# Kernel tuning notes

Hardware: AMD Instinct MI355X
Metric: run time of the kernel (lower is better)

The kernel has to match this reference:

```python
import jax, jax.numpy as jnp
import numpy as np

N = 8192
IN_FEATS = 256
D = IN_FEATS // 4  # 64, bottleneck dim
HID = 64           # MLP hidden_dim
K_MAX = 9
K_EC = 20
SLOPE = 0.01       # torch LeakyReLU default


def _leaky(x):
    return jnp.where(x >= 0, x, SLOPE * x)


def _knn_idx(f, k):
    # f: [N, d]; returns [N, k] indices of k nearest (incl. self, dist 0), ascending distance
    sq = jnp.sum(f * f, axis=1)
    dist = sq[:, None] + sq[None, :] - 2.0 * (f @ f.T)  # [N, N]
    _, idx = jax.lax.top_k(-dist, k)
    return idx


def _edge_conv(f, idx, Wt, bt, Wp, bp, W1, b1, W2, b2):
    # f: [N, d]; idx: [N, k] neighbor (src) indices; dst is the row node.
    x_nb = f[idx]                                   # [N, k, d] gather of src feats
    theta = (f[:, None, :] - x_nb) @ Wt.T + bt      # v_sub_u -> theta Linear
    phi = f @ Wp.T + bp                             # [N, d]
    z = phi[:, None, :] + theta                     # [N, k, d]
    # MLP(hidden=64, 2 layers, leaky_relu, activation_first=True)
    z = _leaky(z) @ W1.T + b1
    z = _leaky(z) @ W2.T + b2
    return jnp.max(z, axis=1)                       # max aggregation per dst


def _lin_init(key, out_dim, in_dim):
    k1, k2 = jax.random.split(key)
    bound = 1.0 / np.sqrt(in_dim)
    W = jax.random.uniform(k1, (out_dim, in_dim), jnp.float32, -bound, bound)
    b = jax.random.uniform(k2, (out_dim,), jnp.float32, -bound, bound)
    return W, b


def setup_inputs() -> dict:
    key = jax.random.key(0)
    keys = jax.random.split(key, 12)
    inp = {"feature": jax.random.normal(keys[0], (N, IN_FEATS), jnp.float32)}
    inp["Wb"], inp["bb"] = _lin_init(keys[1], D, IN_FEATS)
    inp["Wt1"], inp["bt1"] = _lin_init(keys[2], D, D)
    inp["Wp1"], inp["bp1"] = _lin_init(keys[3], D, D)
    inp["Wm1a"], inp["bm1a"] = _lin_init(keys[4], HID, D)
    inp["Wm1b"], inp["bm1b"] = _lin_init(keys[5], D, HID)
    inp["Wt2"], inp["bt2"] = _lin_init(keys[6], D, D)
    inp["Wp2"], inp["bp2"] = _lin_init(keys[7], D, D)
    inp["Wm2a"], inp["bm2a"] = _lin_init(keys[8], HID, D)
    inp["Wm2b"], inp["bm2b"] = _lin_init(keys[9], D, HID)
    inp["Wl"], inp["bl"] = _lin_init(keys[10], IN_FEATS, 3 * D)
    return inp


def reference(feature, Wb, bb, Wt1, bt1, Wp1, bp1, Wm1a, bm1a, Wm1b, bm1b,
              Wt2, bt2, Wp2, bp2, Wm2a, bm2a, Wm2b, bm2b, Wl, bl):
    f = feature @ Wb.T + bb                          # bottleneck [N, D]
    # KNN indices are non-differentiable (torch topk indices) -> stop_gradient
    idx40 = _knn_idx(jax.lax.stop_gradient(f), K_EC * 2)  # 40-NN, ascending distance
    idx9 = idx40[:, :K_MAX]
    idx20 = idx40[:, :K_EC]            # dilation 1
    idx20_d2 = idx40[:, ::2]           # dilation 2: every 2nd of 40-NN
    h_max = jnp.max(f[idx9], axis=1)   # copy_u + max over 9-NN
    h1 = _edge_conv(f, idx20, Wt1, bt1, Wp1, bp1, Wm1a, bm1a, Wm1b, bm1b)
    h2 = _edge_conv(f, idx20_d2, Wt2, bt2, Wp2, bp2, Wm2a, bm2a, Wm2b, bm2b)
    h = jnp.concatenate([h1, h2, h_max], axis=1) @ Wl.T + bl
    return h + feature                 # residual
```

## Files before the change

kernel.cpp:

```cpp
#include <hip/hip_runtime.h>
#include <math.h>

#define NPT   8192
#define FIN   256
#define DD    64
#define KSEL  48
#define SSEG  320

#define LEAKY(x) (((x) >= 0.f) ? (x) : 0.01f*(x))

using short8v = __attribute__((ext_vector_type(8))) short;
using f32x4   = __attribute__((ext_vector_type(4))) float;

__device__ inline unsigned short f2bf(float x) {
  union { float f; unsigned u; } v; v.f = x;
  unsigned r = v.u + 0x7fff + ((v.u >> 16) & 1);
  return (unsigned short)(r >> 16);
}
__device__ inline float bf2f(unsigned short h) {
  union { unsigned u; float f; } v; v.u = ((unsigned)h) << 16; return v.f;
}
__device__ inline unsigned key_of(float f) {
  unsigned u = __float_as_uint(f);
  return (u & 0x80000000u) ? ~u : (u | 0x80000000u);
}
__device__ inline float key_inv(unsigned k) {
  unsigned u = (k >> 31) ? (k ^ 0x80000000u) : ~k;
  return __uint_as_float(u);
}

__global__ void k0_prep(const float* __restrict__ Wl, const float* __restrict__ Wb,
                        const float* __restrict__ Wt1, const float* __restrict__ Wp1,
                        const float* __restrict__ Wt2, const float* __restrict__ Wp2,
                        float* __restrict__ WlT, float* __restrict__ WbT,
                        float* __restrict__ WtT1, float* __restrict__ WpT1,
                        float* __restrict__ WtT2, float* __restrict__ WpT2)
{
  const int b = blockIdx.x, t = threadIdx.x;
  if (b < 192) {
    WlT[b*256 + t] = Wl[t*192 + b];
  } else if (b < 256) {
    int j = (b - 192)*4 + (t >> 6), o = t & 63;
    WbT[j*64 + o] = Wb[o*256 + j];
  } else {
    int m = b - 256;
    const float* src = (m==0) ? Wt1 : (m==1) ? Wp1 : (m==2) ? Wt2 : Wp2;
    float*       dst = (m==0) ? WtT1: (m==1) ? WpT1: (m==2) ? WtT2: WpT2;
    #pragma unroll
    for (int i = 0; i < 16; ++i) {
      int idx = t + 256*i, r = idx >> 6, c = idx & 63;
      dst[c*64 + r] = src[r*64 + c];
    }
  }
}

__global__ __launch_bounds__(256) void k1_precompute(
    const float* __restrict__ feature, const float* __restrict__ WbT, const float* __restrict__ bb,
    const float* __restrict__ WtT1, const float* __restrict__ bt1,
    const float* __restrict__ WpT1, const float* __restrict__ bp1,
    const float* __restrict__ WtT2, const float* __restrict__ bt2,
    const float* __restrict__ WpT2, const float* __restrict__ bp2,
    double* __restrict__ f64d, double* __restrict__ sq64,
    float* __restrict__ f32v, float* __restrict__ sqf,
    float* __restrict__ u1, float* __restrict__ c1,
    float* __restrict__ u2, float* __restrict__ c2)
{
  __shared__ float f_s[4*64];
  const int w = threadIdx.x >> 6, l = threadIdx.x & 63;
  const int i = blockIdx.x*4 + w;
  const float* frow = feature + i*FIN;
  double a0 = (double)bb[l], a1 = 0.0, a2 = 0.0, a3 = 0.0;
  #pragma unroll 2
  for (int j = 0; j < FIN; j += 4) {
    float4 fv = *(const float4*)&frow[j];
    a0 += (double)fv.x * (double)WbT[(j+0)*64 + l];
    a1 += (double)fv.y * (double)WbT[(j+1)*64 + l];
    a2 += (double)fv.z * (double)WbT[(j+2)*64 + l];
    a3 += (double)fv.w * (double)WbT[(j+3)*64 + l];
  }
  double facc = (a0 + a1) + (a2 + a3);
  f64d[i*DD + l] = facc;
  float f32 = (float)facc;
  f32v[i*DD + l] = f32;
  double s = facc*facc;
  #pragma unroll
  for (int off = 32; off; off >>= 1) s += __shfl_xor(s, off);
  if (l == 0) { sq64[i] = s; sqf[i] = (float)s; }
  f_s[w*64 + l] = f32;
  float au1 = 0.f, ap1 = 0.f, au2 = 0.f, ap2 = 0.f;
  for (int e = 0; e < DD; ++e) {
    float fe = f_s[w*64 + e];
    au1 += fe * WtT1[e*64 + l];
    ap1 += fe * WpT1[e*64 + l];
    au2 += fe * WtT2[e*64 + l];
    ap2 += fe * WpT2[e*64 + l];
  }
  u1[i*DD+l] = au1;
  c1[i*DD+l] = ap1 + bp1[l] + au1 + bt1[l];
  u2[i*DD+l] = au2;
  c2[i*DD+l] = ap2 + bp2[l] + au2 + bt2[l];
}

__global__ __launch_bounds__(256) void k1b_frag(
    const float* __restrict__ f32v,
    unsigned short* __restrict__ Saf, unsigned short* __restrict__ Sbf)
{
  const int w = threadIdx.x >> 6, l = threadIdx.x & 63;
  const int task = blockIdx.x*4 + w;
  const int tile = task / 6, ks = task % 6;
  const int row  = tile*16 + (l & 15);
  const int inner = (ks & 1)*32 + ((l >> 4) << 3);
  union { unsigned short u[8]; short8v v; } pa, pb;
  #pragma unroll
  for (int j = 0; j < 8; ++j) {
    float x = f32v[row*64 + inner + j];
    unsigned short hi = f2bf(x);
    unsigned short lo = f2bf(x - bf2f(hi));
    pa.u[j] = (ks < 4) ? hi : lo;
    pb.u[j] = (ks < 2) ? hi : ((ks < 4) ? lo : hi);
  }
  size_t off = ((size_t)(tile*6 + ks)*64 + l)*8;
  *(short8v*)&Saf[off] = pa.v;
  *(short8v*)&Sbf[off] = pb.v;
}

__global__ __launch_bounds__(256) void k1c_wfrag(
    const float* __restrict__ Wm1a, const float* __restrict__ Wm1b,
    const float* __restrict__ Wm2a, const float* __restrict__ Wm2b,
    unsigned short* __restrict__ F1a, unsigned short* __restrict__ F1b,
    unsigned short* __restrict__ F2a, unsigned short* __restrict__ F2b)
{
  const int w = threadIdx.x >> 6, l = threadIdx.x & 63;
  const int task = blockIdx.x*4 + w;
  const int which = task / 24, rem = task % 24;
  const int nt = rem / 6, ks = rem % 6;
  const float* W = (which==0) ? Wm1a : (which==1) ? Wm1b : (which==2) ? Wm2a : Wm2b;
  unsigned short* F = (which==0) ? F1a : (which==1) ? F1b : (which==2) ? F2a : F2b;
  const int row = nt*16 + (l & 15);
  const int inner = (ks & 1)*32 + ((l >> 4) << 3);
  union { unsigned short u[8]; short8v v; } p;
  #pragma unroll
  for (int j = 0; j < 8; ++j) {
    float x = W[row*64 + inner + j];
    unsigned short hi = f2bf(x);
    unsigned short lo = f2bf(x - bf2f(hi));
    p.u[j] = (ks < 2) ? hi : ((ks < 4) ? lo : hi);
  }
  *(short8v*)&F[((size_t)(nt*6 + ks)*64 + l)*8] = p.v;
}

#define MFMA_PAIR6(ACC, AF, BF)                                                  \
  ACC = __builtin_amdgcn_mfma_f32_16x16x32_bf16(AF[0], BF[0], ACC, 0, 0, 0);     \
  ACC = __builtin_amdgcn_mfma_f32_16x16x32_bf16(AF[1], BF[1], ACC, 0, 0, 0);     \
  ACC = __builtin_amdgcn_mfma_f32_16x16x32_bf16(AF[0], BF[2], ACC, 0, 0, 0);     \
  ACC = __builtin_amdgcn_mfma_f32_16x16x32_bf16(AF[1], BF[3], ACC, 0, 0, 0);     \
  ACC = __builtin_amdgcn_mfma_f32_16x16x32_bf16(AF[2], BF[0], ACC, 0, 0, 0);     \
  ACC = __builtin_amdgcn_mfma_f32_16x16x32_bf16(AF[3], BF[1], ACC, 0, 0, 0);

__global__ __launch_bounds__(512) void k2a_sample(
    const unsigned short* __restrict__ Saf,
    const unsigned short* __restrict__ Sbf,
    const float* __restrict__ sqf,
    float* __restrict__ sampD)
{
  const int t = threadIdx.x, w = t >> 6, l = t & 63;
  const int qb = blockIdx.x >> 1, sh = blockIdx.x & 1;
  const int qbase = qb * 32;
  short8v afr[2][4];
  #pragma unroll
  for (int mt = 0; mt < 2; ++mt) {
    const size_t b = (size_t)(qb*2 + mt)*6;
    afr[mt][0] = *(const short8v*)&Saf[((b+0)*64 + l)*8];
    afr[mt][1] = *(const short8v*)&Saf[((b+1)*64 + l)*8];
    afr[mt][2] = *(const short8v*)&Saf[((b+4)*64 + l)*8];
    afr[mt][3] = *(const short8v*)&Saf[((b+5)*64 + l)*8];
  }
  const int ncol = w*16 + (l & 15);
  for (int sl = 0; sl < 4; ++sl) {
    const int s = sh*4 + sl;
    const int cb = s*8;
    const int jbase = cb*128;
    short8v bfr[4];
    {
      const size_t b = (size_t)(cb*8 + w)*6;
      #pragma unroll
      for (int k = 0; k < 4; ++k)
        bfr[k] = *(const short8v*)&Sbf[((b+k)*64 + l)*8];
    }
    const float sc = sqf[jbase + ncol];
    f32x4 acc0 = {0.f,0.f,0.f,0.f}, acc1 = {0.f,0.f,0.f,0.f};
    MFMA_PAIR6(acc0, afr[0], bfr);
    MFMA_PAIR6(acc1, afr[1], bfr);
    #pragma unroll
    for (int r = 0; r < 4; ++r) {
      const int q0 = qbase + 0*16 + (l >> 4)*4 + r;
      const int q1 = qbase + 1*16 + (l >> 4)*4 + r;
      sampD[(size_t)q0*1024 + s*128 + ncol] = sc - 2.0f*acc0[r];
      sampD[(size_t)q1*1024 + s*128 + ncol] = sc - 2.0f*acc1[r];
    }
  }
}

__global__ __launch_bounds__(256) void k2t_threshold(
    const float* __restrict__ sampD, float* __restrict__ Tq)
{
  const int w = threadIdx.x >> 6, l = threadIdx.x & 63;
  const int q = blockIdx.x*4 + w;
  unsigned ku[16];
  #pragma unroll
  for (int k = 0; k < 16; ++k)
    ku[k] = key_of(sampD[(size_t)q*1024 + k*64 + l]);
  unsigned prefix = 0; int need = 41;
  for (int b = 31; b >= 0; --b) {
    unsigned p2 = prefix << 1;
    int c = 0;
    #pragma unroll
    for (int k = 0; k < 16; ++k) c += ((ku[k] >> b) == p2);
    #pragma unroll
    for (int off = 32; off; off >>= 1) c += __shfl_xor(c, off);
    if (c >= need) prefix = p2; else { prefix = p2 | 1u; need -= c; }
  }
  if (l == 0) Tq[q] = key_inv(prefix);
}

__global__ __launch_bounds__(512) void k2f_filter(
    const unsigned short* __restrict__ Saf,
    const unsigned short* __restrict__ Sbf,
    const float* __restrict__ sqf,
    const float* __restrict__ Tq,
    int* __restrict__ cnt_g,
    float* __restrict__ survD, int* __restrict__ survI)
{
  __shared__ int cnt_sh[32];
  const int t = threadIdx.x, w = t >> 6, l = t & 63;
  const int qb = blockIdx.x >> 1, half = blockIdx.x & 1;
  const int qbase = qb * 32;
  if (t < 32) cnt_sh[t] = 0;
  short8v afr[2][4];
  float Tr[2][4]; int qloc[2][4];
  #pragma unroll
  for (int mt = 0; mt < 2; ++mt) {
    const size_t b = (size_t)(qb*2 + mt)*6;
    afr[mt][0] = *(const short8v*)&Saf[((b+0)*64 + l)*8];
    afr[mt][1] = *(const short8v*)&Saf[((b+1)*64 + l)*8];
    afr[mt][2] = *(const short8v*)&Saf[((b+4)*64 + l)*8];
    afr[mt][3] = *(const short8v*)&Saf[((b+5)*64 + l)*8];
    #pragma unroll
    for (int r = 0; r < 4; ++r) {
      qloc[mt][r] = mt*16 + (l >> 4)*4 + r;
      Tr[mt][r] = Tq[qbase + qloc[mt][r]];
    }
  }
  short8v bfr[4];
  {
    const size_t b = (size_t)(half*256 + w)*6;
    #pragma unroll
    for (int k = 0; k < 4; ++k)
      bfr[k] = *(const short8v*)&Sbf[((b+k)*64 + l)*8];
  }
  const int ncol = w*16 + (l & 15);
  __syncthreads();
  for (int cb = 0; cb < 32; ++cb) {
    const int jbase = half*4096 + cb*128;
    const float sc = sqf[jbase + ncol];
    f32x4 acc0 = {0.f,0.f,0.f,0.f}, acc1 = {0.f,0.f,0.f,0.f};
    MFMA_PAIR6(acc0, afr[0], bfr);
    MFMA_PAIR6(acc1, afr[1], bfr);
    if (cb < 31) {
      const size_t b = (size_t)(half*256 + (cb+1)*8 + w)*6;
      #pragma unroll
      for (int k = 0; k < 4; ++k)
        bfr[k] = *(const short8v*)&Sbf[((b+k)*64 + l)*8];
    }
    const int j = jbase + ncol;
    #pragma unroll
    for (int r = 0; r < 4; ++r) {
      float d0 = sc - 2.0f*acc0[r];
      if (d0 < Tr[0][r]) {
        int slot = atomicAdd(&cnt_sh[qloc[0][r]], 1);
        if (slot < SSEG) {
          size_t base = ((size_t)(qbase + qloc[0][r])*2 + half)*SSEG + slot;
          survD[base] = d0; survI[base] = j;
        }
      }
      float d1 = sc - 2.0f*acc1[r];
      if (d1 < Tr[1][r]) {
        int slot = atomicAdd(&cnt_sh[qloc[1][r]], 1);
        if (slot < SSEG) {
          size_t base = ((size_t)(qbase + qloc[1][r])*2 + half)*SSEG + slot;
          survD[base] = d1; survI[base] = j;
        }
      }
    }
  }
  __syncthreads();
  if (t < 32) cnt_g[(qbase + t)*2 + half] = cnt_sh[t];
}

__global__ __launch_bounds__(256) void k2s_select(
    const float* __restrict__ survD, const int* __restrict__ survI,
    const int* __restrict__ cnt_g, int* __restrict__ idx48)
{
  const int w = threadIdx.x >> 6, l = threadIdx.x & 63;
  const int node = blockIdx.x*4 + w;
  const int c0 = min(cnt_g[node*2 + 0], SSEG);
  const int c1 = min(cnt_g[node*2 + 1], SSEG);
  unsigned ku[10]; int iv[10];
  #pragma unroll
  for (int k = 0; k < 10; ++k) {
    int e = k*64 + l;
    int seg = (e >= SSEG);
    int off = e - seg*SSEG;
    bool v = off < (seg ? c1 : c0);
    size_t base = ((size_t)node*2 + seg)*SSEG + off;
    float d = v ? survD[base] : 0.f;
    iv[k] = v ? survI[base] : 0;
    ku[k] = v ? key_of(d) : 0xFFFFFFFFu;
  }
  unsigned prefix = 0; int need = KSEL;
  for (int b = 31; b >= 0; --b) {
    unsigned p2 = prefix << 1;
    int c = 0;
    #pragma unroll
    for (int k = 0; k < 10; ++k) c += ((ku[k] >> b) == p2);
    #pragma unroll
    for (int off = 32; off; off >>= 1) c += __shfl_xor(c, off);
    if (c >= need) prefix = p2; else { prefix = p2 | 1u; need -= c; }
  }
  const unsigned long long below = (1ull << l) - 1ull;
  int base = 0;
  #pragma unroll
  for (int k = 0; k < 10; ++k) {
    unsigned long long blt = __ballot(ku[k] < prefix);
    if (ku[k] < prefix) {
      int pos = base + __popcll(blt & below);
      idx48[(size_t)node*KSEL + pos] = iv[k];
    }
    base += __popcll(blt);
  }
  #pragma unroll
  for (int k = 0; k < 10; ++k) {
    unsigned long long beq = __ballot(ku[k] == prefix);
    if (ku[k] == prefix) {
      int pos = base + __popcll(beq & below);
      if (pos < KSEL) idx48[(size_t)node*KSEL + pos] = iv[k];
    }
    base += __popcll(beq);
  }
}

__global__ __launch_bounds__(256) void k2r_rerank(
    const double* __restrict__ f64d, const double* __restrict__ sq64,
    const int* __restrict__ idx48, int* __restrict__ idx40)
{
  __shared__ double part[KSEL][4];
  __shared__ double dist_sh[KSEL];
  __shared__ int    cand_sh[KSEL];
  const int t = threadIdx.x;
  const int node = blockIdx.x;
  if (t < KSEL) cand_sh[t] = idx48[(size_t)node*KSEL + t];
  __syncthreads();
  if (t < 192) {
    int c = t >> 2, qt = t & 3;
    int cand = cand_sh[c];
    const double* fi = f64d + (size_t)node*DD + qt*16;
    const double* fc = f64d + (size_t)cand*DD + qt*16;
    double a0 = 0.0, a1 = 0.0;
    #pragma unroll
    for (int d = 0; d < 16; d += 2) { a0 += fi[d]*fc[d]; a1 += fi[d+1]*fc[d+1]; }
    part[c][qt] = a0 + a1;
  }
  __syncthreads();
  if (t < KSEL) {
    int cand = cand_sh[t];
    dist_sh[t] = sq64[node] + sq64[cand]
               - 2.0*(part[t][0] + part[t][1] + part[t][2] + part[t][3]);
  }
  __syncthreads();
  if (t < KSEL) {
    double dm = dist_sh[t]; int cand = cand_sh[t];
    int rank = 0;
    for (int j = 0; j < KSEL; ++j) {
      double dj = dist_sh[j];
      int    ij = cand_sh[j];
      rank += (dj < dm) || (dj == dm && ij < cand);
    }
    if (rank < 40) idx40[(size_t)node*40 + rank] = cand;
  }
}

__global__ __launch_bounds__(256) void k3_edgeconv(
    const float* __restrict__ f32v,
    const float* __restrict__ u1, const float* __restrict__ c1,
    const float* __restrict__ u2, const float* __restrict__ c2,
    const unsigned short* __restrict__ F1a, const unsigned short* __restrict__ F1b,
    const unsigned short* __restrict__ F2a, const unsigned short* __restrict__ F2b,
    const float* __restrict__ bm1a, const float* __restrict__ bm1b,
    const float* __restrict__ bm2a, const float* __restrict__ bm2b,
    const int* __restrict__ idx40, float* __restrict__ hout)
{
  __shared__ unsigned short au16[2][32*72];
  __shared__ float red_s[2][2][64];
  __shared__ int idx_sh[80];
  const int t = threadIdx.x;
  const int w = t >> 6, l = t & 63;
  const int sub = w >> 1, mt = w & 1;
  const int i = blockIdx.x*2 + sub;
  const int row16 = l & 15;
  const int q8 = (l >> 4) << 3;
  if (t < 80) idx_sh[t] = idx40[(size_t)(blockIdx.x*2 + (t >= 40))*40 + (t >= 40 ? t - 40 : t)];
  __syncthreads();

  for (int conv = 0; conv < 2; ++conv) {
    const float* u_g = conv ? u2 : u1;
    const float* c_g = conv ? c2 : c1;
    const unsigned short* WfA = conv ? F2a : F1a;
    const unsigned short* WfB = conv ? F2b : F1b;
    const float* bav = conv ? bm2a : bm1a;
    const float* bbv = conv ? bm2b : bm1b;

    const int row = mt*16 + row16;
    const bool valid = row < 20;
    const int nb = valid ? idx_sh[sub*40 + (conv ? 2*row : row)] : idx_sh[sub*40];
    short8v fr0, fr1;
    {
      const float* up = u_g + (size_t)nb*DD;
      const float* cp = c_g + (size_t)i*DD;
      float4 ua = *(const float4*)&up[q8];
      float4 ub = *(const float4*)&up[q8 + 4];
      float4 uc = *(const float4*)&up[32 + q8];
      float4 ud = *(const float4*)&up[32 + q8 + 4];
      float4 ca = *(const float4*)&cp[q8];
      float4 cb = *(const float4*)&cp[q8 + 4];
      float4 cc = *(const float4*)&cp[32 + q8];
      float4 cd = *(const float4*)&cp[32 + q8 + 4];
      float z0[8] = {ca.x-ua.x, ca.y-ua.y, ca.z-ua.z, ca.w-ua.w,
                     cb.x-ub.x, cb.y-ub.y, cb.z-ub.z, cb.w-ub.w};
      float z1[8] = {cc.x-uc.x, cc.y-uc.y, cc.z-uc.z, cc.w-uc.w,
                     cd.x-ud.x, cd.y-ud.y, cd.z-ud.z, cd.w-ud.w};
      union { unsigned short us[8]; short8v v; } h0, h1;
      #pragma unroll
      for (int j = 0; j < 8; ++j) {
        float x0 = valid ? LEAKY(z0[j]) : 0.f;
        float x1 = valid ? LEAKY(z1[j]) : 0.f;
        h0.us[j] = f2bf(x0);
        h1.us[j] = f2bf(x1);
      }
      fr0 = h0.v; fr1 = h1.v;
    }
    f32x4 acc[4] = {{0,0,0,0},{0,0,0,0},{0,0,0,0},{0,0,0,0}};
    #pragma unroll
    for (int nt = 0; nt < 4; ++nt) {
      const unsigned short* p = WfA + (size_t)nt*6*64*8;
      short8v w0 = *(const short8v*)&p[(0*64 + l)*8];
      short8v w1 = *(const short8v*)&p[(1*64 + l)*8];
      acc[nt] = __builtin_amdgcn_mfma_f32_16x16x32_bf16(fr0, w0, acc[nt], 0, 0, 0);
      acc[nt] = __builtin_amdgcn_mfma_f32_16x16x32_bf16(fr1, w1, acc[nt], 0, 0, 0);
    }
    #pragma unroll
    for (int nt = 0; nt < 4; ++nt) {
      const int col = nt*16 + row16;
      const float ba = bav[col];
      #pragma unroll
      for (int r = 0; r < 4; ++r) {
        const int arow = mt*16 + (l >> 4)*4 + r;
        float v = acc[nt][r] + ba; v = LEAKY(v);
        au16[sub][arow*72 + col] = f2bf(v);
      }
    }
    __syncthreads();
    short8v g0, g1;
    {
      const unsigned short* base = &au16[sub][(mt*16 + row16)*72 + q8];
      g0 = *(const short8v*)&base[0];
      g1 = *(const short8v*)&base[32];
    }
    f32x4 bacc[4] = {{0,0,0,0},{0,0,0,0},{0,0,0,0},{0,0,0,0}};
    #pragma unroll
    for (int nt = 0; nt < 4; ++nt) {
      const unsigned short* p = WfB + (size_t)nt*6*64*8;
      short8v w0 = *(const short8v*)&p[(0*64 + l)*8];
      short8v w1 = *(const short8v*)&p[(1*64 + l)*8];
      bacc[nt] = __builtin_amdgcn_mfma_f32_16x16x32_bf16(g0, w0, bacc[nt], 0, 0, 0);
      bacc[nt] = __builtin_amdgcn_mfma_f32_16x16x32_bf16(g1, w1, bacc[nt], 0, 0, 0);
    }
    #pragma unroll
    for (int nt = 0; nt < 4; ++nt) {
      const int col = nt*16 + row16;
      const float bb2 = bbv[col];
      float m = -__builtin_inff();
      #pragma unroll
      for (int r = 0; r < 4; ++r) {
        const int arow = mt*16 + (l >> 4)*4 + r;
        if (arow < 20) m = fmaxf(m, bacc[nt][r] + bb2);
      }
      m = fmaxf(m, __shfl_xor(m, 16));
      m = fmaxf(m, __shfl_xor(m, 32));
      if ((l >> 4) == 0) red_s[sub][mt][col] = m;
    }
    __syncthreads();
    if (t < 128) {
      int s2 = t >> 6, col = t & 63;
      hout[(size_t)(blockIdx.x*2 + s2)*192 + conv*64 + col] =
          fmaxf(red_s[s2][0][col], red_s[s2][1][col]);
    }
    __syncthreads();
  }
  if (t < 128) {
    int s2 = t >> 6, col = t & 63;
    float m = -__builtin_inff();
    #pragma unroll
    for (int k = 0; k < 9; ++k)
      m = fmaxf(m, f32v[(size_t)idx_sh[s2*40 + k]*DD + col]);
    hout[(size_t)(blockIdx.x*2 + s2)*192 + 128 + col] = m;
  }
}

__global__ __launch_bounds__(256) void k4_final(
    const float* __restrict__ hbuf, const float* __restrict__ WlT,
    const float* __restrict__ bl, const float* __restrict__ feature,
    float* __restrict__ out)
{
  __shared__ __align__(16) float h_sh[16*192];
  const int t = threadIdx.x;
  const int nbase = blockIdx.x * 16;
  #pragma unroll
  for (int r = 0; r < 3; ++r) {
    int flat = t + 256*r;
    int n = flat / 48, j4 = flat % 48;
    *(float4*)&h_sh[n*192 + 4*j4] = *(const float4*)&hbuf[(nbase+n)*192 + 4*j4];
  }
  __syncthreads();
  float acc[16];
  #pragma unroll
  for (int n = 0; n < 16; ++n) acc[n] = 0.f;
  for (int j4 = 0; j4 < 48; ++j4) {
    float w0 = WlT[(4*j4+0)*256 + t];
    float w1 = WlT[(4*j4+1)*256 + t];
    float w2 = WlT[(4*j4+2)*256 + t];
    float w3 = WlT[(4*j4+3)*256 + t];
    #pragma unroll
    for (int n = 0; n < 16; ++n) {
      float4 hv = *(const float4*)&h_sh[n*192 + 4*j4];
      acc[n] += hv.x*w0 + hv.y*w1 + hv.z*w2 + hv.w*w3;
    }
  }
  float blv = bl[t];
  #pragma unroll
  for (int n = 0; n < 16; ++n)
    out[(nbase+n)*256 + t] = acc[n] + blv + feature[(nbase+n)*256 + t];
}

extern "C" void kernel_launch(void* const* d_in, const int* in_sizes, int n_in,
                              void* d_out, int out_size, void* d_ws, size_t ws_size,
                              hipStream_t stream) {
  const float* feature = (const float*)d_in[0];
  const float* Wb   = (const float*)d_in[1];
  const float* bb   = (const float*)d_in[2];
  const float* Wt1  = (const float*)d_in[3];
  const float* bt1  = (const float*)d_in[4];
  const float* Wp1  = (const float*)d_in[5];
  const float* bp1  = (const float*)d_in[6];
  const float* Wm1a = (const float*)d_in[7];
  const float* bm1a = (const float*)d_in[8];
  const float* Wm1b = (const float*)d_in[9];
  const float* bm1b = (const float*)d_in[10];
  const float* Wt2  = (const float*)d_in[11];
  const float* bt2  = (const float*)d_in[12];
  const float* Wp2  = (const float*)d_in[13];
  const float* bp2  = (const float*)d_in[14];
  const float* Wm2a = (const float*)d_in[15];
  const float* bm2a = (const float*)d_in[16];
  const float* Wm2b = (const float*)d_in[17];
  const float* bm2b = (const float*)d_in[18];
  const float* Wl   = (const float*)d_in[19];
  const float* bl   = (const float*)d_in[20];
  float* out = (float*)d_out;

  char* ws = (char*)d_ws;
  double* f64d = (double*)(ws + 0);
  double* sq64 = (double*)(ws + 4194304);
  float*  f32v = (float*)(ws + 4259840);
  float*  sqf  = (float*)(ws + 6356992);
  float*  u1   = (float*)(ws + 6389760);
  float*  c1   = (float*)(ws + 8486912);
  float*  u2   = (float*)(ws + 10584064);
  float*  c2   = (float*)(ws + 12681216);
  int*    idx48= (int*)(ws + 14778368);
  int*    idx40= (int*)(ws + 16351232);
  float*  hbuf = (float*)(ws + 17661952);
  float*  WlT  = (float*)(ws + 23953408);
  unsigned short* Saf = (unsigned short*)(ws + 24150016);
  unsigned short* Sbf = (unsigned short*)(ws + 27295744);
  float*  WbT  = (float*)(ws + 30441472);
  float*  WtT1 = (float*)(ws + 30507008);
  float*  WpT1 = (float*)(ws + 30523392);
  float*  WtT2 = (float*)(ws + 30539776);
  float*  WpT2 = (float*)(ws + 30556160);
  unsigned short* F1a = (unsigned short*)(ws + 30572544);
  unsigned short* F1b = (unsigned short*)(ws + 30597120);
  unsigned short* F2a = (unsigned short*)(ws + 30621696);
  unsigned short* F2b = (unsigned short*)(ws + 30646272);
  float*  Tq   = (float*)(ws + 30670848);
  int*    cnt_g= (int*)(ws + 30703616);
  float*  survD= (float*)(ws + 30769152);
  int*    survI= (int*)(ws + 51740672);
  float*  sampD= (float*)(ws + 30769152);

  hipLaunchKernelGGL(k0_prep, dim3(260), dim3(256), 0, stream,
                     Wl, Wb, Wt1, Wp1, Wt2, Wp2, WlT, WbT, WtT1, WpT1, WtT2, WpT2);
  hipLaunchKernelGGL(k1c_wfrag, dim3(24), dim3(256), 0, stream,
                     Wm1a, Wm1b, Wm2a, Wm2b, F1a, F1b, F2a, F2b);
  hipLaunchKernelGGL(k1_precompute, dim3(2048), dim3(256), 0, stream,
                     feature, WbT, bb, WtT1, bt1, WpT1, bp1, WtT2, bt2, WpT2, bp2,
                     f64d, sq64, f32v, sqf, u1, c1, u2, c2);
  hipLaunchKernelGGL(k1b_frag, dim3(768), dim3(256), 0, stream, f32v, Saf, Sbf);
  hipLaunchKernelGGL(k2a_sample, dim3(512), dim3(512), 0, stream, Saf, Sbf, sqf, sampD);
  hipLaunchKernelGGL(k2t_threshold, dim3(2048), dim3(256), 0, stream, sampD, Tq);
  hipLaunchKernelGGL(k2f_filter, dim3(512), dim3(512), 0, stream,
                     Saf, Sbf, sqf, Tq, cnt_g, survD, survI);
  hipLaunchKernelGGL(k2s_select, dim3(2048), dim3(256), 0, stream, survD, survI, cnt_g, idx48);
  hipLaunchKernelGGL(k2r_rerank, dim3(8192), dim3(256), 0, stream, f64d, sq64, idx48, idx40);
  hipLaunchKernelGGL(k3_edgeconv, dim3(4096), dim3(256), 0, stream,
                     f32v, u1, c1, u2, c2, F1a, F1b, F2a, F2b,
                     bm1a, bm1b, bm2a, bm2b, idx40, hbuf);
  hipLaunchKernelGGL(k4_final, dim3(512), dim3(256), 0, stream, hbuf, WlT, bl, feature, out);
}
```

Measured before the change: 396.7 us.

## Split precompute: stage bottleneck weights in LDS, compute theta/phi projections via MFMA

The old fused precompute kernel is split in two. The new first kernel computes the f64 bottleneck projection with 8 rows per block and the WbT weights staged in shared memory as float4. The u/c projections (Wt and Wt+Wp, folded algebraically) now run as a bf16 hi/lo split MFMA kernel that reuses the Saf fragments, after the KNN stages. This replaces scalar fp32 FMA loops and their global weight reads with matrix-core work. The cost is some precision, since the split bf16 scheme drops the lo*lo terms, and the new G weight buffers alias the f64d workspace region, which is only safe because they are written after rerank.

```diff
diff --git a/kernel.cpp b/kernel.cpp
--- a/kernel.cpp
+++ b/kernel.cpp
@@ -30,75 +30,57 @@
 }
 
 __global__ void k0_prep(const float* __restrict__ Wl, const float* __restrict__ Wb,
-                        const float* __restrict__ Wt1, const float* __restrict__ Wp1,
-                        const float* __restrict__ Wt2, const float* __restrict__ Wp2,
-                        float* __restrict__ WlT, float* __restrict__ WbT,
-                        float* __restrict__ WtT1, float* __restrict__ WpT1,
-                        float* __restrict__ WtT2, float* __restrict__ WpT2)
+                        float* __restrict__ WlT, float* __restrict__ WbT)
 {
   const int b = blockIdx.x, t = threadIdx.x;
   if (b < 192) {
     WlT[b*256 + t] = Wl[t*192 + b];
-  } else if (b < 256) {
+  } else {
     int j = (b - 192)*4 + (t >> 6), o = t & 63;
     WbT[j*64 + o] = Wb[o*256 + j];
-  } else {
-    int m = b - 256;
-    const float* src = (m==0) ? Wt1 : (m==1) ? Wp1 : (m==2) ? Wt2 : Wp2;
-    float*       dst = (m==0) ? WtT1: (m==1) ? WpT1: (m==2) ? WtT2: WpT2;
-    #pragma unroll
-    for (int i = 0; i < 16; ++i) {
-      int idx = t + 256*i, r = idx >> 6, c = idx & 63;
-      dst[c*64 + r] = src[r*64 + c];
-    }
-  }
-}
-
-__global__ __launch_bounds__(256) void k1_precompute(
-    const float* __restrict__ feature, const float* __restrict__ WbT, const float* __restrict__ bb,
-    const float* __restrict__ WtT1, const float* __restrict__ bt1,
-    const float* __restrict__ WpT1, const float* __restrict__ bp1,
-    const float* __restrict__ WtT2, const float* __restrict__ bt2,
-    const float* __restrict__ WpT2, const float* __restrict__ bp2,
+  }
+}
+
+__global__ __launch_bounds__(512) void k1a_f64(
+    const float* __restrict__ feature, const float* __restrict__ WbT,
+    const float* __restrict__ bb,
     double* __restrict__ f64d, double* __restrict__ sq64,
-    float* __restrict__ f32v, float* __restrict__ sqf,
-    float* __restrict__ u1, float* __restrict__ c1,
-    float* __restrict__ u2, float* __restrict__ c2)
-{
-  __shared__ float f_s[4*64];
-  const int w = threadIdx.x >> 6, l = threadIdx.x & 63;
-  const int i = blockIdx.x*4 + w;
-  const float* frow = feature + i*FIN;
+    float* __restrict__ f32v, float* __restrict__ sqf)
+{
+  __shared__ __align__(16) float4 Q[64*64];
+  const int t = threadIdx.x, w = t >> 6, l = t & 63;
+  const int i = blockIdx.x*8 + w;
+  #pragma unroll
+  for (int r = 0; r < 8; ++r) {
+    int flat = t + 512*r;
+    int jj = flat >> 6, col = flat & 63;
+    float4 q;
+    q.x = WbT[(4*jj+0)*64 + col];
+    q.y = WbT[(4*jj+1)*64 + col];
+    q.z = WbT[(4*jj+2)*64 + col];
+    q.w = WbT[(4*jj+3)*64 + col];
+    Q[jj*64 + col] = q;
+  }
+  __syncthreads();
+  const float* frow = feature + (size_t)i*FIN;
   double a0 = (double)bb[l], a1 = 0.0, a2 = 0.0, a3 = 0.0;
-  #pragma unroll 2
-  for (int j = 0; j < FIN; j += 4) {
-    float4 fv = *(const float4*)&frow[j];
-    a0 += (double)fv.x * (double)WbT[(j+0)*64 + l];
-    a1 += (double)fv.y * (double)WbT[(j+1)*64 + l];
-    a2 += (double)fv.z * (double)WbT[(j+2)*64 + l];
-    a3 += (double)fv.w * (double)WbT[(j+3)*64 + l];
+  #pragma unroll 4
+  for (int jj = 0; jj < 64; ++jj) {
+    float4 fv = *(const float4*)&frow[4*jj];
+    float4 q = Q[jj*64 + l];
+    a0 += (double)fv.x * (double)q.x;
+    a1 += (double)fv.y * (double)q.y;
+    a2 += (double)fv.z * (double)q.z;
+    a3 += (double)fv.w * (double)q.w;
   }
   double facc = (a0 + a1) + (a2 + a3);
-  f64d[i*DD + l] = facc;
+  f64d[(size_t)i*DD + l] = facc;
   float f32 = (float)facc;
-  f32v[i*DD + l] = f32;
+  f32v[(size_t)i*DD + l] = f32;
   double s = facc*facc;
   #pragma unroll
   for (int off = 32; off; off >>= 1) s += __shfl_xor(s, off);
   if (l == 0) { sq64[i] = s; sqf[i] = (float)s; }
-  f_s[w*64 + l] = f32;
-  float au1 = 0.f, ap1 = 0.f, au2 = 0.f, ap2 = 0.f;
-  for (int e = 0; e < DD; ++e) {
-    float fe = f_s[w*64 + e];
-    au1 += fe * WtT1[e*64 + l];
-    ap1 += fe * WpT1[e*64 + l];
-    au2 += fe * WtT2[e*64 + l];
-    ap2 += fe * WpT2[e*64 + l];
-  }
-  u1[i*DD+l] = au1;
-  c1[i*DD+l] = ap1 + bp1[l] + au1 + bt1[l];
-  u2[i*DD+l] = au2;
-  c2[i*DD+l] = ap2 + bp2[l] + au2 + bt2[l];
 }
 
 __global__ __launch_bounds__(256) void k1b_frag(
@@ -127,26 +109,86 @@
 __global__ __launch_bounds__(256) void k1c_wfrag(
     const float* __restrict__ Wm1a, const float* __restrict__ Wm1b,
     const float* __restrict__ Wm2a, const float* __restrict__ Wm2b,
+    const float* __restrict__ Wt1, const float* __restrict__ Wp1,
+    const float* __restrict__ Wt2, const float* __restrict__ Wp2,
     unsigned short* __restrict__ F1a, unsigned short* __restrict__ F1b,
-    unsigned short* __restrict__ F2a, unsigned short* __restrict__ F2b)
+    unsigned short* __restrict__ F2a, unsigned short* __restrict__ F2b,
+    unsigned short* __restrict__ Gu1, unsigned short* __restrict__ Gc1,
+    unsigned short* __restrict__ Gu2, unsigned short* __restrict__ Gc2)
 {
   const int w = threadIdx.x >> 6, l = threadIdx.x & 63;
   const int task = blockIdx.x*4 + w;
   const int which = task / 24, rem = task % 24;
   const int nt = rem / 6, ks = rem % 6;
-  const float* W = (which==0) ? Wm1a : (which==1) ? Wm1b : (which==2) ? Wm2a : Wm2b;
-  unsigned short* F = (which==0) ? F1a : (which==1) ? F1b : (which==2) ? F2a : F2b;
+  const float* W  = (which==0) ? Wm1a : (which==1) ? Wm1b : (which==2) ? Wm2a :
+                    (which==3) ? Wm2b : (which==4) ? Wt1  : (which==5) ? Wt1  :
+                    (which==6) ? Wt2  : Wt2;
+  const float* W2 = (which==5) ? Wp1 : (which==7) ? Wp2 : (const float*)0;
+  unsigned short* F = (which==0) ? F1a : (which==1) ? F1b : (which==2) ? F2a :
+                      (which==3) ? F2b : (which==4) ? Gu1 : (which==5) ? Gc1 :
+                      (which==6) ? Gu2 : Gc2;
   const int row = nt*16 + (l & 15);
   const int inner = (ks & 1)*32 + ((l >> 4) << 3);
   union { unsigned short u[8]; short8v v; } p;
   #pragma unroll
   for (int j = 0; j < 8; ++j) {
     float x = W[row*64 + inner + j];
+    if (W2) x += W2[row*64 + inner + j];
     unsigned short hi = f2bf(x);
     unsigned short lo = f2bf(x - bf2f(hi));
     p.u[j] = (ks < 2) ? hi : ((ks < 4) ? lo : hi);
   }
   *(short8v*)&F[((size_t)(nt*6 + ks)*64 + l)*8] = p.v;
+}
+
+__global__ __launch_bounds__(256) void k1d_uc(
+    const unsigned short* __restrict__ Saf,
+    const unsigned short* __restrict__ Gu1, const unsigned short* __restrict__ Gc1,
+    const unsigned short* __restrict__ Gu2, const unsigned short* __restrict__ Gc2,
+    const float* __restrict__ bt1, const float* __restrict__ bp1,
+    const float* __restrict__ bt2, const float* __restrict__ bp2,
+    float* __restrict__ u1, float* __restrict__ c1,
+    float* __restrict__ u2, float* __restrict__ c2)
+{
+  const int t = threadIdx.x, w = t >> 6, l = t & 63;
+  const int tile = blockIdx.x*4 + w;
+  short8v ah0, ah1, al0, al1;
+  {
+    const size_t b = (size_t)tile*6;
+    ah0 = *(const short8v*)&Saf[((b+0)*64 + l)*8];
+    ah1 = *(const short8v*)&Saf[((b+1)*64 + l)*8];
+    al0 = *(const short8v*)&Saf[((b+4)*64 + l)*8];
+    al1 = *(const short8v*)&Saf[((b+5)*64 + l)*8];
+  }
+  const int row0 = tile*16 + (l >> 4)*4;
+  const int c16 = l & 15;
+  #pragma unroll
+  for (int m = 0; m < 4; ++m) {
+    const unsigned short* G = (m==0) ? Gu1 : (m==1) ? Gc1 : (m==2) ? Gu2 : Gc2;
+    float* outp = (m==0) ? u1 : (m==1) ? c1 : (m==2) ? u2 : c2;
+    #pragma unroll
+    for (int nt = 0; nt < 4; ++nt) {
+      const unsigned short* p = G + (size_t)nt*6*64*8;
+      short8v wh0 = *(const short8v*)&p[(0*64 + l)*8];
+      short8v wh1 = *(const short8v*)&p[(1*64 + l)*8];
+      short8v wl0 = *(const short8v*)&p[(2*64 + l)*8];
+      short8v wl1 = *(const short8v*)&p[(3*64 + l)*8];
+      f32x4 acc = {0.f, 0.f, 0.f, 0.f};
+      acc = __builtin_amdgcn_mfma_f32_16x16x32_bf16(ah0, wh0, acc, 0, 0, 0);
+      acc = __builtin_amdgcn_mfma_f32_16x16x32_bf16(ah1, wh1, acc, 0, 0, 0);
+      acc = __builtin_amdgcn_mfma_f32_16x16x32_bf16(ah0, wl0, acc, 0, 0, 0);
+      acc = __builtin_amdgcn_mfma_f32_16x16x32_bf16(ah1, wl1, acc, 0, 0, 0);
+      acc = __builtin_amdgcn_mfma_f32_16x16x32_bf16(al0, wh0, acc, 0, 0, 0);
+      acc = __builtin_amdgcn_mfma_f32_16x16x32_bf16(al1, wh1, acc, 0, 0, 0);
+      const int col = nt*16 + c16;
+      float bias = 0.f;
+      if (m == 1) bias = bt1[col] + bp1[col];
+      if (m == 3) bias = bt2[col] + bp2[col];
+      #pragma unroll
+      for (int r = 0; r < 4; ++r)
+        outp[(size_t)(row0 + r)*64 + col] = acc[r] + bias;
+    }
+  }
 }
 
 #define MFMA_PAIR6(ACC, AF, BF)                                                  \
@@ -593,10 +635,6 @@
   unsigned short* Saf = (unsigned short*)(ws + 24150016);
   unsigned short* Sbf = (unsigned short*)(ws + 27295744);
   float*  WbT  = (float*)(ws + 30441472);
-  float*  WtT1 = (float*)(ws + 30507008);
-  float*  WpT1 = (float*)(ws + 30523392);
-  float*  WtT2 = (float*)(ws + 30539776);
-  float*  WpT2 = (float*)(ws + 30556160);
   unsigned short* F1a = (unsigned short*)(ws + 30572544);
   unsigned short* F1b = (unsigned short*)(ws + 30597120);
   unsigned short* F2a = (unsigned short*)(ws + 30621696);
@@ -606,14 +644,14 @@
   float*  survD= (float*)(ws + 30769152);
   int*    survI= (int*)(ws + 51740672);
   float*  sampD= (float*)(ws + 30769152);
-
-  hipLaunchKernelGGL(k0_prep, dim3(260), dim3(256), 0, stream,
-                     Wl, Wb, Wt1, Wp1, Wt2, Wp2, WlT, WbT, WtT1, WpT1, WtT2, WpT2);
-  hipLaunchKernelGGL(k1c_wfrag, dim3(24), dim3(256), 0, stream,
-                     Wm1a, Wm1b, Wm2a, Wm2b, F1a, F1b, F2a, F2b);
-  hipLaunchKernelGGL(k1_precompute, dim3(2048), dim3(256), 0, stream,
-                     feature, WbT, bb, WtT1, bt1, WpT1, bp1, WtT2, bt2, WpT2, bp2,
-                     f64d, sq64, f32v, sqf, u1, c1, u2, c2);
+  unsigned short* Gu1 = (unsigned short*)(ws + 0);
+  unsigned short* Gc1 = (unsigned short*)(ws + 24576);
+  unsigned short* Gu2 = (unsigned short*)(ws + 49152);
+  unsigned short* Gc2 = (unsigned short*)(ws + 73728);
+
+  hipLaunchKernelGGL(k0_prep, dim3(256), dim3(256), 0, stream, Wl, Wb, WlT, WbT);
+  hipLaunchKernelGGL(k1a_f64, dim3(1024), dim3(512), 0, stream,
+                     feature, WbT, bb, f64d, sq64, f32v, sqf);
   hipLaunchKernelGGL(k1b_frag, dim3(768), dim3(256), 0, stream, f32v, Saf, Sbf);
   hipLaunchKernelGGL(k2a_sample, dim3(512), dim3(512), 0, stream, Saf, Sbf, sqf, sampD);
   hipLaunchKernelGGL(k2t_threshold, dim3(2048), dim3(256), 0, stream, sampD, Tq);
@@ -621,6 +659,11 @@
                      Saf, Sbf, sqf, Tq, cnt_g, survD, survI);
   hipLaunchKernelGGL(k2s_select, dim3(2048), dim3(256), 0, stream, survD, survI, cnt_g, idx48);
   hipLaunchKernelGGL(k2r_rerank, dim3(8192), dim3(256), 0, stream, f64d, sq64, idx48, idx40);
+  hipLaunchKernelGGL(k1c_wfrag, dim3(48), dim3(256), 0, stream,
+                     Wm1a, Wm1b, Wm2a, Wm2b, Wt1, Wp1, Wt2, Wp2,
+                     F1a, F1b, F2a, F2b, Gu1, Gc1, Gu2, Gc2);
+  hipLaunchKernelGGL(k1d_uc, dim3(128), dim3(256), 0, stream,
+                     Saf, Gu1, Gc1, Gu2, Gc2, bt1, bp1, bt2, bp2, u1, c1, u2, c2);
   hipLaunchKernelGGL(k3_edgeconv, dim3(4096), dim3(256), 0, stream,
                      f32v, u1, c1, u2, c2, F1a, F1b, F2a, F2b,
                      bm1a, bm1b, bm2a, bm2b, idx40, hbuf);
```

After: 378.7 us. 1.05x faster.
